# Performance work log

Measured on AMD Instinct MI355X. Metric: run time of the kernel, lower is better.

The kernel has to match this reference:

```python
import jax, jax.numpy as jnp
import numpy as np

N_NODES = 50000
N_EDGES = 1600000
D_IN = 512
D_HEAD = 64
N_HEADS_L1 = 4


def _segment_mean(data, seg_ids, num_segments, counts):
    s = jax.ops.segment_sum(data, seg_ids, num_segments=num_segments)
    denom = jnp.maximum(counts, 1.0)
    return jnp.where(counts[:, None] > 0, s / denom[:, None], 0.0)


def setup_inputs() -> dict:
    key = jax.random.key(0)
    k1, k2, k3, k4 = jax.random.split(key, 4)
    node_features = jax.random.normal(k1, (N_NODES, D_IN), dtype=jnp.float32)
    edge_index = jax.random.randint(k2, (2, N_EDGES), 0, N_NODES, dtype=jnp.int32)
    W1 = jax.random.normal(k3, (N_HEADS_L1, D_IN, D_HEAD), dtype=jnp.float32) * (1.0 / np.sqrt(D_IN))
    W2 = jax.random.normal(k4, (N_HEADS_L1 * D_HEAD, D_HEAD), dtype=jnp.float32) * (1.0 / np.sqrt(N_HEADS_L1 * D_HEAD))
    return {"node_features": node_features, "edge_index": edge_index, "W1": W1, "W2": W2}


def reference(node_features, edge_index, W1, W2):
    n = node_features.shape[0]
    src = edge_index[0]  # segment ids (destination of aggregation in TF code)
    dst = edge_index[1]  # gathered neighbors
    counts = jax.ops.segment_sum(jnp.ones_like(src, dtype=node_features.dtype), src, num_segments=n)

    # Layer 1: 4 heads, Dense(64, no bias) -> gather(dst) -> unsorted_segment_mean(src) -> concat -> elu
    head_outs = []
    for i in range(N_HEADS_L1):
        t = node_features @ W1[i]                 # (N, 64)
        agg = _segment_mean(t[dst], src, n, counts)  # (N, 64)
        head_outs.append(agg)
    h = jax.nn.elu(jnp.concatenate(head_outs, axis=-1))  # (N, 256)

    # Layer 2: 1 head, linear activation
    t2 = h @ W2                                   # (N, 64)
    out = _segment_mean(t2[dst], src, n, counts)  # (N, 64)
    return out
```

## Files before the change

### kernel.cpp

```cpp
#include <hip/hip_runtime.h>
#include <hip/hip_bf16.h>
#include <stdint.h>

#define N_NODES 50000
#define N_EDGES 1600000
#define D_IN    512
#define D_H1    256
#define D_OUT   64

#define NBUK    196
#define MAXB    9216
#define EPB     4096
#define NPB     391
#define SLOT    96

#define NR      50001
#define ZROW    50000

typedef __attribute__((ext_vector_type(8))) short  short8;
typedef __attribute__((ext_vector_type(4))) float  f32x4;
typedef __attribute__((ext_vector_type(2))) float  f32x2;
typedef __attribute__((ext_vector_type(4))) unsigned int u32x4;
typedef __attribute__((ext_vector_type(2))) unsigned int u32x2;

typedef __attribute__((address_space(1))) void GASV;
typedef __attribute__((address_space(3))) void LASV;

static __device__ __forceinline__ unsigned short f2bf(float f) {
    union { float f; unsigned int u; } c; c.f = f;
    unsigned int u = c.u;
    return (unsigned short)((u + 0x7FFFu + ((u >> 16) & 1u)) >> 16);
}
static __device__ __forceinline__ unsigned int cvtpk(float a, float b) {
    unsigned int r;
    asm("v_cvt_pk_bf16_f32 %0, %1, %2" : "=v"(r) : "v"(a), "v"(b));
    return r;
}
static __device__ __forceinline__ unsigned short f2bf1(float f) {
    return (unsigned short)cvtpk(f, f);
}
static __device__ __forceinline__ float uasf(unsigned int u) {
    union { unsigned int u; float f; } c; c.u = u; return c.f;
}
static __device__ __forceinline__ void glds16(const unsigned int* g, unsigned int* l) {
    __builtin_amdgcn_global_load_lds((GASV*)g, (LASV*)l, 16, 0, 0);
}


__global__ __launch_bounds__(256) void part_kernel(const int* __restrict__ src,
                                                   const int* __restrict__ dst,
                                                   int* __restrict__ gcnt,
                                                   unsigned int* __restrict__ gbuk) {
    __shared__ int hist[NBUK];
    __shared__ int lofs[NBUK];
    __shared__ int gbase[NBUK];
    __shared__ int sbuf[256];
    __shared__ unsigned int sorted[EPB];
    __shared__ unsigned char bid[EPB];

    const int t  = threadIdx.x;
    const int e0 = blockIdx.x * EPB;
    int ec = N_EDGES - e0; if (ec > EPB) ec = EPB;

    for (int i = t; i < NBUK; i += 256) hist[i] = 0;
    __syncthreads();

    unsigned int rec[16];
    int bb[16], idx[16];
#pragma unroll
    for (int j = 0; j < 16; ++j) {
        int i = j * 256 + t;
        if (i < ec) {
            int s = src[e0 + i], d = dst[e0 + i];
            int b = s >> 8;
            rec[j] = ((unsigned int)(s & 255) << 16) | (unsigned int)d;
            bb[j]  = b;
            idx[j] = atomicAdd(&hist[b], 1);
        } else bb[j] = -1;
    }
    __syncthreads();

    int v = (t < NBUK) ? hist[t] : 0;
    sbuf[t] = v;
    __syncthreads();
#pragma unroll
    for (int off = 1; off < 256; off <<= 1) {
        int x = (t >= off) ? sbuf[t - off] : 0;
        __syncthreads();
        sbuf[t] += x;
        __syncthreads();
    }
    if (t < NBUK) {
        lofs[t]  = sbuf[t] - v;
        gbase[t] = atomicAdd(&gcnt[t], v);
    }
    __syncthreads();

#pragma unroll
    for (int j = 0; j < 16; ++j) {
        if (bb[j] >= 0) {
            int p = lofs[bb[j]] + idx[j];
            sorted[p] = rec[j];
            bid[p] = (unsigned char)bb[j];
        }
    }
    __syncthreads();

    for (int i = t; i < ec; i += 256) {
        int b = bid[i];
        int p = gbase[b] + (i - lofs[b]);
        gbuk[(size_t)b * MAXB + p] = sorted[i];
    }
}


__global__ __launch_bounds__(256) void sort_kernel(const int* __restrict__ gcnt,
                                                   const unsigned int* __restrict__ gbuk,
                                                   unsigned short* __restrict__ sdst,
                                                   int* __restrict__ deg) {
    __shared__ int hist[256];
    __shared__ int nofs[256];
    __shared__ int sbuf[256];
    __shared__ unsigned short list[MAXB];

    const int t = threadIdx.x;
    const int b = blockIdx.x;
    const int cnt = gcnt[b];
    const unsigned int* buk = gbuk + (size_t)b * MAXB;

    hist[t] = 0;
    __syncthreads();
    for (int i = t; i < cnt; i += 256)
        atomicAdd(&hist[buk[i] >> 16], 1);
    __syncthreads();

    int v = hist[t];
    sbuf[t] = v;
    __syncthreads();
#pragma unroll
    for (int off = 1; off < 256; off <<= 1) {
        int x = (t >= off) ? sbuf[t - off] : 0;
        __syncthreads();
        sbuf[t] += x;
        __syncthreads();
    }
    nofs[t] = sbuf[t] - v;
    const int n = b * 256 + t;
    if (n < N_NODES) deg[n] = v;
    __syncthreads();

    for (int i = t; i < cnt; i += 256) {
        unsigned int r = buk[i];
        int p = atomicAdd(&nofs[r >> 16], 1);
        list[p] = (unsigned short)(r & 0xffffu);
    }
    __syncthreads();

    for (int base = 0; base < 256; base += 32) {
        int node = base + (t >> 3);
        int l8   = t & 7;
        int vv   = hist[node];
        int beg  = nofs[node] - vv;
        int n2   = b * 256 + node;
        if (n2 < N_NODES) {
            int words = ((vv + 7) & ~7) >> 1;
            if (words == 0) words = 4;
            unsigned int* out32 = (unsigned int*)(sdst + (size_t)n2 * SLOT);
            for (int j2 = l8; j2 < words; j2 += 8) {
                unsigned int lo = (2 * j2     < vv) ? list[beg + 2 * j2]     : (unsigned int)ZROW;
                unsigned int hi = (2 * j2 + 1 < vv) ? list[beg + 2 * j2 + 1] : (unsigned int)ZROW;
                out32[j2] = lo | (hi << 16);
            }
        }
    }
}


__global__ void convw_kernel(const float* __restrict__ W1, const float* __restrict__ W2,
                             unsigned short* __restrict__ Bt1, unsigned short* __restrict__ Bt2,
                             unsigned short* __restrict__ t1, unsigned short* __restrict__ t2) {
    int i = blockIdx.x * 256 + threadIdx.x;
    if (i < 4 * 512 * 64) {
        int h = i >> 15;
        int k = (i >> 6) & 511;
        int j = i & 63;
        Bt1[(h * 64 + j) * 512 + k] = f2bf(W1[i]);
    } else if (i < 4 * 512 * 64 + 256 * 64) {
        int r = i - 4 * 512 * 64;
        int k = r >> 6;
        int n = r & 63;
        Bt2[n * 256 + k] = f2bf(W2[r]);
    } else {
        int r = i - (4 * 512 * 64 + 256 * 64);
        if (r < 256) {
            t1[(size_t)ZROW * 256 + r] = 0;
        } else if (r < 256 + 64) {
            t2[(size_t)ZROW * 64 + (r - 256)] = 0;
        }
    }
}


__global__ __launch_bounds__(512) void gemm1_kernel(const float* __restrict__ A,
                                                    const unsigned short* __restrict__ Bt,
                                                    unsigned short* __restrict__ C) {
    constexpr int BM = 128, BK = 32, LDK = 40, K = D_IN, M = N_NODES;
    __shared__ unsigned short As[BM * LDK];
    __shared__ unsigned short Bs[256 * LDK];

    const int tid  = threadIdx.x;
    const int lane = tid & 63;
    const int w    = tid >> 6;
    const int wm   = (w >> 2) * 64;
    const int wn   = (w & 3) * 64;
    const int quad = lane >> 4;
    const int l15  = lane & 15;
    const int bm   = blockIdx.x;

    f32x4 acc[4][4];
#pragma unroll
    for (int mi = 0; mi < 4; ++mi)
#pragma unroll
        for (int ni = 0; ni < 4; ++ni)
            acc[mi][ni] = (f32x4){0.f, 0.f, 0.f, 0.f};

    const int r0 = tid >> 2;
    const int f8 = tid & 3;

    for (int k0 = 0; k0 < K; k0 += BK) {
        {
            int grow = bm * BM + r0;
            if (grow >= M) grow = M - 1;
            const float* ap = A + (size_t)grow * K + k0 + f8 * 8;
            f32x4 v0 = *(const f32x4*)ap;
            f32x4 v1 = *(const f32x4*)(ap + 4);
            u32x4 pk;
            pk[0] = cvtpk(v0[0], v0[1]);
            pk[1] = cvtpk(v0[2], v0[3]);
            pk[2] = cvtpk(v1[0], v1[1]);
            pk[3] = cvtpk(v1[2], v1[3]);
            *(u32x4*)&As[r0 * LDK + f8 * 8] = pk;
        }
        {
#pragma unroll
            for (int p = 0; p < 2; ++p) {
                int row = p * 128 + r0;
                u32x4 v = *(const u32x4*)(Bt + (size_t)row * K + k0 + f8 * 8);
                *(u32x4*)&Bs[row * LDK + f8 * 8] = v;
            }
        }
        __syncthreads();

        short8 af[4], bfr[4];
#pragma unroll
        for (int mi = 0; mi < 4; ++mi)
            af[mi] = *(const short8*)&As[(wm + mi * 16 + l15) * LDK + quad * 8];
#pragma unroll
        for (int ni = 0; ni < 4; ++ni)
            bfr[ni] = *(const short8*)&Bs[(wn + ni * 16 + l15) * LDK + quad * 8];
#pragma unroll
        for (int mi = 0; mi < 4; ++mi)
#pragma unroll
            for (int ni = 0; ni < 4; ++ni)
                acc[mi][ni] = __builtin_amdgcn_mfma_f32_16x16x32_bf16(af[mi], bfr[ni], acc[mi][ni], 0, 0, 0);
        __syncthreads();
    }

#pragma unroll
    for (int mi = 0; mi < 4; ++mi) {
        int row0 = bm * BM + wm + mi * 16 + quad * 4;
#pragma unroll
        for (int ni = 0; ni < 4; ++ni) {
            int col = wn + ni * 16 + l15;
#pragma unroll
            for (int r = 0; r < 4; ++r) {
                int row = row0 + r;
                if (row < M) C[(size_t)row * 256 + col] = f2bf1(acc[mi][ni][r]);
            }
        }
    }
}


__global__ __launch_bounds__(256) void aggf_kernel(const unsigned short* __restrict__ t1,
                                                   const int* __restrict__ deg,
                                                   const unsigned short* __restrict__ sdst,
                                                   const unsigned short* __restrict__ Bt2,
                                                   unsigned short* __restrict__ t2) {
    __shared__ __align__(16) unsigned int ring[4][2][1024];
    __shared__ __align__(16) unsigned short h_lds[16][264];

    const int w    = __builtin_amdgcn_readfirstlane(threadIdx.x >> 6);
    const int lane = threadIdx.x & 63;
    const int s0b  = blockIdx.x * 16;
    const int s0   = s0b + w * 4;
    const unsigned int* tb32 = (const unsigned int*)t1;
    const unsigned int loff = ((unsigned)(lane & 31)) << 2;

    const int end0 = deg[s0 + 0], end1 = deg[s0 + 1], end2 = deg[s0 + 2], end3 = deg[s0 + 3];
    const int elv0 = sdst[(size_t)(s0 + 0) * SLOT + lane];
    const int elv1 = sdst[(size_t)(s0 + 1) * SLOT + lane];
    const int elv2 = sdst[(size_t)(s0 + 2) * SLOT + lane];
    const int elv3 = sdst[(size_t)(s0 + 3) * SLOT + lane];
    asm volatile("" :: "v"(end0), "v"(end1), "v"(end2), "v"(end3),
                       "v"(elv0), "v"(elv1), "v"(elv2), "v"(elv3));

    const int nch0 = end0 ? (end0 + 7) >> 3 : 1;
    const int nch1 = end1 ? (end1 + 7) >> 3 : 1;
    const int nch2 = end2 ? (end2 + 7) >> 3 : 1;
    const int nch3 = end3 ? (end3 + 7) >> 3 : 1;

#define AGGF_ISSUE(ELV, C, B)                                                           \
    {                                                                                   \
        int q  = ((C) << 3) + (lane >> 5);                                              \
        int ra = __shfl(ELV, q);                                                        \
        int rb_ = __shfl(ELV, q + 2);                                                   \
        int rc = __shfl(ELV, q + 4);                                                    \
        int rd = __shfl(ELV, q + 6);                                                    \
        unsigned int* dp = &ring[w][B][0];                                              \
        glds16(tb32 + (unsigned)ra  * 128u + loff, dp);                                 \
        glds16(tb32 + (unsigned)rb_ * 128u + loff, dp + 256);                           \
        glds16(tb32 + (unsigned)rc  * 128u + loff, dp + 512);                           \
        glds16(tb32 + (unsigned)rd  * 128u + loff, dp + 768);                           \
    }

#define AGGF_CONS(B)                                                                    \
    {                                                                                   \
        const unsigned int* rbp = &ring[w][B][lane << 1];                               \
        _Pragma("unroll")                                                               \
        for (int r = 0; r < 8; ++r) {                                                   \
            u32x2 v = *(const u32x2*)(rbp + (r << 7));                                  \
            a0 += uasf(v[0] << 16); a1 += uasf(v[0] & 0xffff0000u);                     \
            a2 += uasf(v[1] << 16); a3 += uasf(v[1] & 0xffff0000u);                     \
        }                                                                               \
    }

#define AGGF_EPI(J)                                                                     \
    {                                                                                   \
        float iv = (end##J > 0) ? (1.0f / (float)end##J) : 0.f;                         \
        float m0 = a0 * iv, m1 = a1 * iv, m2 = a2 * iv, m3 = a3 * iv;                   \
        m0 = (m0 > 0.f) ? m0 : (__expf(m0) - 1.f);                                      \
        m1 = (m1 > 0.f) ? m1 : (__expf(m1) - 1.f);                                      \
        m2 = (m2 > 0.f) ? m2 : (__expf(m2) - 1.f);                                      \
        m3 = (m3 > 0.f) ? m3 : (__expf(m3) - 1.f);                                      \
        u32x2 hw;                                                                       \
        hw[0] = cvtpk(m0, m1);                                                          \
        hw[1] = cvtpk(m2, m3);                                                          \
        *(u32x2*)&h_lds[(w << 2) + J][lane << 2] = hw;                                  \
        a0 = a1 = a2 = a3 = 0.f;                                                        \
    }

#define WAIT4 asm volatile("s_waitcnt vmcnt(4)" ::: "memory"); __builtin_amdgcn_sched_barrier(0);

    float a0 = 0.f, a1 = 0.f, a2 = 0.f, a3 = 0.f;
    int gb = 0;

    AGGF_ISSUE(elv0, 0, 0); ++gb;
    for (int c = 1; c < nch0; ++c) {
        int b = gb & 1; AGGF_ISSUE(elv0, c, b); ++gb; WAIT4; AGGF_CONS(b ^ 1);
    }
    { int b = gb & 1; AGGF_ISSUE(elv1, 0, b); ++gb; WAIT4; AGGF_CONS(b ^ 1); AGGF_EPI(0); }
    for (int c = 1; c < nch1; ++c) {
        int b = gb & 1; AGGF_ISSUE(elv1, c, b); ++gb; WAIT4; AGGF_CONS(b ^ 1);
    }
    { int b = gb & 1; AGGF_ISSUE(elv2, 0, b); ++gb; WAIT4; AGGF_CONS(b ^ 1); AGGF_EPI(1); }
    for (int c = 1; c < nch2; ++c) {
        int b = gb & 1; AGGF_ISSUE(elv2, c, b); ++gb; WAIT4; AGGF_CONS(b ^ 1);
    }
    { int b = gb & 1; AGGF_ISSUE(elv3, 0, b); ++gb; WAIT4; AGGF_CONS(b ^ 1); AGGF_EPI(2); }
    for (int c = 1; c < nch3; ++c) {
        int b = gb & 1; AGGF_ISSUE(elv3, c, b); ++gb; WAIT4; AGGF_CONS(b ^ 1);
    }
    asm volatile("s_waitcnt vmcnt(0)" ::: "memory");
    __builtin_amdgcn_sched_barrier(0);
    { int b = (gb & 1) ^ 1; AGGF_CONS(b); AGGF_EPI(3); }

    __syncthreads();

    {
        const int l15 = lane & 15, quad = lane >> 4;
        f32x4 acc = (f32x4){0.f, 0.f, 0.f, 0.f};
#pragma unroll
        for (int st = 0; st < 8; ++st) {
            short8 afr = *(const short8*)&h_lds[l15][st * 32 + quad * 8];
            short8 bfr = *(const short8*)(Bt2 + (size_t)(w * 16 + l15) * 256 + st * 32 + quad * 8);
            acc = __builtin_amdgcn_mfma_f32_16x16x32_bf16(afr, bfr, acc, 0, 0, 0);
        }
#pragma unroll
        for (int r = 0; r < 4; ++r)
            t2[(size_t)(s0b + quad * 4 + r) * 64 + w * 16 + l15] = f2bf1(acc[r]);
    }
}


__global__ __launch_bounds__(256) void agg2_kernel(const unsigned short* __restrict__ t2,
                                                   const int* __restrict__ deg,
                                                   const unsigned short* __restrict__ sdst,
                                                   float* __restrict__ out) {
    __shared__ __align__(16) unsigned int ring[4][2][256];

    const int w    = __builtin_amdgcn_readfirstlane(threadIdx.x >> 6);
    const int lane = threadIdx.x & 63;
    const int s0   = blockIdx.x * 16 + w * 4;
    const unsigned int* tb32 = (const unsigned int*)t2;
    const unsigned int loff = ((unsigned)(lane & 7)) << 2;

    const int end0 = deg[s0 + 0], end1 = deg[s0 + 1], end2 = deg[s0 + 2], end3 = deg[s0 + 3];
    const int elv0 = sdst[(size_t)(s0 + 0) * SLOT + lane];
    const int elv1 = sdst[(size_t)(s0 + 1) * SLOT + lane];
    const int elv2 = sdst[(size_t)(s0 + 2) * SLOT + lane];
    const int elv3 = sdst[(size_t)(s0 + 3) * SLOT + lane];
    asm volatile("" :: "v"(end0), "v"(end1), "v"(end2), "v"(end3),
                       "v"(elv0), "v"(elv1), "v"(elv2), "v"(elv3));

#define AGG2_ISSUE(ELV, D, B)                                                           \
    {                                                                                   \
        int r = __shfl(ELV, ((D) << 3) + (lane >> 3));                                  \
        glds16(tb32 + (unsigned)r * 32u + loff, &ring[w][B][0]);                        \
    }

#define AGG2_CONSUME(B)                                                                 \
    {                                                                                   \
        const unsigned int* rbp = &ring[w][B][lane & 31];                               \
        _Pragma("unroll")                                                               \
        for (int i = 0; i < 4; ++i) {                                                   \
            unsigned int v = rbp[(((i << 1) + (lane >> 5)) << 5)];                      \
            a0 += uasf(v << 16); a1 += uasf(v & 0xffff0000u);                           \
        }                                                                               \
    }

#define AGG2_NODE(J)                                                                    \
    {                                                                                   \
        const int end = end##J;                                                         \
        const int nch = ((end + 7) & ~7) >> 3;                                          \
        float a0 = 0.f, a1 = 0.f;                                                       \
        if (nch > 0) {                                                                  \
            AGG2_ISSUE(elv##J, 0, 0);                                                   \
            for (int d = 1; d < nch; ++d) {                                             \
                AGG2_ISSUE(elv##J, d, d & 1);                                           \
                asm volatile("s_waitcnt vmcnt(1)" ::: "memory");                        \
                __builtin_amdgcn_sched_barrier(0);                                      \
                AGG2_CONSUME((d - 1) & 1);                                              \
            }                                                                           \
            asm volatile("s_waitcnt vmcnt(0)" ::: "memory");                            \
            __builtin_amdgcn_sched_barrier(0);                                          \
            AGG2_CONSUME((nch - 1) & 1);                                                \
        }                                                                               \
        a0 += __shfl_xor(a0, 32);                                                       \
        a1 += __shfl_xor(a1, 32);                                                       \
        if (lane < 32) {                                                                \
            float iv = (end > 0) ? (1.0f / (float)end) : 0.f;                           \
            f32x2 rr; rr.x = a0 * iv; rr.y = a1 * iv;                                   \
            *(f32x2*)(out + (size_t)(s0 + J) * D_OUT + (lane & 31) * 2) = rr;           \
        }                                                                               \
    }

    AGG2_NODE(0);
    AGG2_NODE(1);
    AGG2_NODE(2);
    AGG2_NODE(3);
}


extern "C" void kernel_launch(void* const* d_in, const int* in_sizes, int n_in,
                              void* d_out, int out_size, void* d_ws, size_t ws_size,
                              hipStream_t stream) {
    const float* X  = (const float*)d_in[0];
    const int*   ei = (const int*)d_in[1];
    const float* W1 = (const float*)d_in[2];
    const float* W2 = (const float*)d_in[3];
    const int* src = ei;
    const int* dst = ei + N_EDGES;

    char* ws = (char*)d_ws;
    size_t off = 0;
    auto alloc = [&](size_t bytes) {
        off = (off + 255) & ~(size_t)255;
        void* p = ws + off;
        off += bytes;
        return p;
    };
    int*          gcnt = (int*)alloc((size_t)NBUK * 4);
    unsigned int* gbuk = (unsigned int*)alloc((size_t)NBUK * MAXB * 4);
    unsigned short* sdst = (unsigned short*)alloc(((size_t)N_NODES * SLOT + 64) * 2);
    int*          deg  = (int*)alloc((size_t)N_NODES * 4);
    unsigned short* Bt1 = (unsigned short*)alloc((size_t)D_H1 * D_IN * 2);
    unsigned short* Bt2 = (unsigned short*)alloc((size_t)D_OUT * D_H1 * 2);
    unsigned short* t1  = (unsigned short*)alloc((size_t)NR * D_H1 * 2);
    unsigned short* t2  = (unsigned short*)alloc((size_t)NR * D_OUT * 2);

    hipMemsetAsync(gcnt, 0, (size_t)NBUK * 4, stream);

    part_kernel<<<NPB, 256, 0, stream>>>(src, dst, gcnt, gbuk);
    sort_kernel<<<NBUK, 256, 0, stream>>>(gcnt, gbuk, sdst, deg);
    convw_kernel<<<(4 * 512 * 64 + 256 * 64 + 256 + 64 + 255) / 256, 256, 0, stream>>>(
        W1, W2, Bt1, Bt2, t1, t2);

    gemm1_kernel<<<(N_NODES + 127) / 128, 512, 0, stream>>>(X, Bt1, t1);
    aggf_kernel<<<N_NODES / 16, 256, 0, stream>>>(t1, deg, sdst, Bt2, t2);
    agg2_kernel<<<N_NODES / 16, 256, 0, stream>>>(t2, deg, sdst, (float*)d_out);
}
```

Before: 351.8 us.

## Merge partition with weight conversion and sort with GEMM1 into shared launches

Folds the weight-conversion work into the edge partition launch and runs the per-bucket sort alongside the first GEMM in one launch, with blocks dispatched by index. This cuts the launch count from six to four and lets independent stages share the GPU at the same time. To fit the 256-thread combined kernel, the GEMM tile is reduced from 128 to 64 rows with four waves, so each block reuses the B tile less and B is loaded more often overall. The shared memory buffer is sized to the larger of the two bodies, which may lower occupancy for the sort blocks.

```diff
diff --git a/kernel.cpp b/kernel.cpp
--- a/kernel.cpp
+++ b/kernel.cpp
@@ -17,6 +17,9 @@
 #define NR      50001
 #define ZROW    50000
 
+#define NCONVW  578
+#define NGEMM1  782
+
 typedef __attribute__((ext_vector_type(8))) short  short8;
 typedef __attribute__((ext_vector_type(4))) float  f32x4;
 typedef __attribute__((ext_vector_type(2))) float  f32x2;
@@ -47,10 +50,16 @@
 }
 
 
-__global__ __launch_bounds__(256) void part_kernel(const int* __restrict__ src,
-                                                   const int* __restrict__ dst,
-                                                   int* __restrict__ gcnt,
-                                                   unsigned int* __restrict__ gbuk) {
+__global__ __launch_bounds__(256) void pc_kernel(const int* __restrict__ src,
+                                                 const int* __restrict__ dst,
+                                                 int* __restrict__ gcnt,
+                                                 unsigned int* __restrict__ gbuk,
+                                                 const float* __restrict__ W1,
+                                                 const float* __restrict__ W2,
+                                                 unsigned short* __restrict__ Bt1,
+                                                 unsigned short* __restrict__ Bt2,
+                                                 unsigned short* __restrict__ t1,
+                                                 unsigned short* __restrict__ t2) {
     __shared__ int hist[NBUK];
     __shared__ int lofs[NBUK];
     __shared__ int gbase[NBUK];
@@ -58,7 +67,31 @@
     __shared__ unsigned int sorted[EPB];
     __shared__ unsigned char bid[EPB];
 
-    const int t  = threadIdx.x;
+    const int t = threadIdx.x;
+
+    if (blockIdx.x >= NPB) {
+        int i = (blockIdx.x - NPB) * 256 + t;
+        if (i < 4 * 512 * 64) {
+            int h = i >> 15;
+            int k = (i >> 6) & 511;
+            int j = i & 63;
+            Bt1[(h * 64 + j) * 512 + k] = f2bf(W1[i]);
+        } else if (i < 4 * 512 * 64 + 256 * 64) {
+            int r = i - 4 * 512 * 64;
+            int k = r >> 6;
+            int n = r & 63;
+            Bt2[n * 256 + k] = f2bf(W2[r]);
+        } else {
+            int r = i - (4 * 512 * 64 + 256 * 64);
+            if (r < 256) {
+                t1[(size_t)ZROW * 256 + r] = 0;
+            } else if (r < 256 + 64) {
+                t2[(size_t)ZROW * 64 + (r - 256)] = 0;
+            }
+        }
+        return;
+    }
+
     const int e0 = blockIdx.x * EPB;
     int ec = N_EDGES - e0; if (ec > EPB) ec = EPB;
 
@@ -114,14 +147,15 @@
 }
 
 
-__global__ __launch_bounds__(256) void sort_kernel(const int* __restrict__ gcnt,
-                                                   const unsigned int* __restrict__ gbuk,
-                                                   unsigned short* __restrict__ sdst,
-                                                   int* __restrict__ deg) {
-    __shared__ int hist[256];
-    __shared__ int nofs[256];
-    __shared__ int sbuf[256];
-    __shared__ unsigned short list[MAXB];
+static __device__ __forceinline__ void sort_body(char* smem,
+                                                 const int* __restrict__ gcnt,
+                                                 const unsigned int* __restrict__ gbuk,
+                                                 unsigned short* __restrict__ sdst,
+                                                 int* __restrict__ deg) {
+    int* hist = (int*)smem;
+    int* nofs = hist + 256;
+    int* sbuf = nofs + 256;
+    unsigned short* list = (unsigned short*)(sbuf + 256);
 
     const int t = threadIdx.x;
     const int b = blockIdx.x;
@@ -175,47 +209,20 @@
     }
 }
 
-
-__global__ void convw_kernel(const float* __restrict__ W1, const float* __restrict__ W2,
-                             unsigned short* __restrict__ Bt1, unsigned short* __restrict__ Bt2,
-                             unsigned short* __restrict__ t1, unsigned short* __restrict__ t2) {
-    int i = blockIdx.x * 256 + threadIdx.x;
-    if (i < 4 * 512 * 64) {
-        int h = i >> 15;
-        int k = (i >> 6) & 511;
-        int j = i & 63;
-        Bt1[(h * 64 + j) * 512 + k] = f2bf(W1[i]);
-    } else if (i < 4 * 512 * 64 + 256 * 64) {
-        int r = i - 4 * 512 * 64;
-        int k = r >> 6;
-        int n = r & 63;
-        Bt2[n * 256 + k] = f2bf(W2[r]);
-    } else {
-        int r = i - (4 * 512 * 64 + 256 * 64);
-        if (r < 256) {
-            t1[(size_t)ZROW * 256 + r] = 0;
-        } else if (r < 256 + 64) {
-            t2[(size_t)ZROW * 64 + (r - 256)] = 0;
-        }
-    }
-}
-
-
-__global__ __launch_bounds__(512) void gemm1_kernel(const float* __restrict__ A,
-                                                    const unsigned short* __restrict__ Bt,
-                                                    unsigned short* __restrict__ C) {
-    constexpr int BM = 128, BK = 32, LDK = 40, K = D_IN, M = N_NODES;
-    __shared__ unsigned short As[BM * LDK];
-    __shared__ unsigned short Bs[256 * LDK];
+static __device__ __forceinline__ void gemm1_body(char* smem, int bm,
+                                                  const float* __restrict__ A,
+                                                  const unsigned short* __restrict__ Bt,
+                                                  unsigned short* __restrict__ C) {
+    constexpr int BM = 64, BK = 32, LDK = 40, K = D_IN, M = N_NODES;
+    unsigned short* As = (unsigned short*)smem;
+    unsigned short* Bs = As + BM * LDK;
 
     const int tid  = threadIdx.x;
     const int lane = tid & 63;
     const int w    = tid >> 6;
-    const int wm   = (w >> 2) * 64;
-    const int wn   = (w & 3) * 64;
+    const int wn   = w * 64;
     const int quad = lane >> 4;
     const int l15  = lane & 15;
-    const int bm   = blockIdx.x;
 
     f32x4 acc[4][4];
 #pragma unroll
@@ -243,8 +250,8 @@
         }
         {
 #pragma unroll
-            for (int p = 0; p < 2; ++p) {
-                int row = p * 128 + r0;
+            for (int p = 0; p < 4; ++p) {
+                int row = p * 64 + r0;
                 u32x4 v = *(const u32x4*)(Bt + (size_t)row * K + k0 + f8 * 8);
                 *(u32x4*)&Bs[row * LDK + f8 * 8] = v;
             }
@@ -254,7 +261,7 @@
         short8 af[4], bfr[4];
 #pragma unroll
         for (int mi = 0; mi < 4; ++mi)
-            af[mi] = *(const short8*)&As[(wm + mi * 16 + l15) * LDK + quad * 8];
+            af[mi] = *(const short8*)&As[(mi * 16 + l15) * LDK + quad * 8];
 #pragma unroll
         for (int ni = 0; ni < 4; ++ni)
             bfr[ni] = *(const short8*)&Bs[(wn + ni * 16 + l15) * LDK + quad * 8];
@@ -268,7 +275,7 @@
 
 #pragma unroll
     for (int mi = 0; mi < 4; ++mi) {
-        int row0 = bm * BM + wm + mi * 16 + quad * 4;
+        int row0 = bm * BM + mi * 16 + quad * 4;
 #pragma unroll
         for (int ni = 0; ni < 4; ++ni) {
             int col = wn + ni * 16 + l15;
@@ -279,6 +286,18 @@
             }
         }
     }
+}
+
+__global__ __launch_bounds__(256) void sg_kernel(const int* __restrict__ gcnt,
+                                                 const unsigned int* __restrict__ gbuk,
+                                                 unsigned short* __restrict__ sdst,
+                                                 int* __restrict__ deg,
+                                                 const float* __restrict__ A,
+                                                 const unsigned short* __restrict__ Bt,
+                                                 unsigned short* __restrict__ C) {
+    __shared__ __align__(16) char smem[25600];
+    if (blockIdx.x < NBUK) sort_body(smem, gcnt, gbuk, sdst, deg);
+    else                   gemm1_body(smem, blockIdx.x - NBUK, A, Bt, C);
 }
 
 
@@ -491,12 +510,8 @@
 
     hipMemsetAsync(gcnt, 0, (size_t)NBUK * 4, stream);
 
-    part_kernel<<<NPB, 256, 0, stream>>>(src, dst, gcnt, gbuk);
-    sort_kernel<<<NBUK, 256, 0, stream>>>(gcnt, gbuk, sdst, deg);
-    convw_kernel<<<(4 * 512 * 64 + 256 * 64 + 256 + 64 + 255) / 256, 256, 0, stream>>>(
-        W1, W2, Bt1, Bt2, t1, t2);
-
-    gemm1_kernel<<<(N_NODES + 127) / 128, 512, 0, stream>>>(X, Bt1, t1);
+    pc_kernel<<<NPB + NCONVW, 256, 0, stream>>>(src, dst, gcnt, gbuk, W1, W2, Bt1, Bt2, t1, t2);
+    sg_kernel<<<NBUK + NGEMM1, 256, 0, stream>>>(gcnt, gbuk, sdst, deg, X, Bt1, t1);
     aggf_kernel<<<N_NODES / 16, 256, 0, stream>>>(t1, deg, sdst, Bt2, t2);
     agg2_kernel<<<N_NODES / 16, 256, 0, stream>>>(t2, deg, sdst, (float*)d_out);
 }
```

New measurement: 337.1 us. 1.04x faster.
